# Kernel tuning notes

Measured on AMD Instinct MI355X. Metric: run time of the kernel, lower is better.

The kernel has to match this reference:

```python
import jax, jax.numpy as jnp
import numpy as np

KERNEL = 3
GROUP = 8


def setup_inputs() -> dict:
    key = jax.random.key(0)
    k1, k2 = jax.random.split(key)
    x = jax.random.normal(k1, (8, 64, 256, 256), dtype=jnp.float32)
    # 1x1 conv weight (out=group*k^2, in=dim), kaiming-ish scale
    conv_w = jax.random.normal(k2, (GROUP * KERNEL ** 2, 64), dtype=jnp.float32) * 0.1
    return {"x": x, "conv_w": conv_w}


def reference(x, conv_w):
    k, g = KERNEL, GROUP
    n, c, h, w = x.shape
    cg = c // g
    pad = k // 2

    # GAP -> 1x1 conv -> tanh : per-sample, per-group k*k dynamic filter
    gap = x.mean(axis=(2, 3))                                   # (n, c)
    filt = jnp.einsum('nc,oc->no', gap, conv_w)                 # (n, g*k*k)
    filt = jnp.tanh(filt).reshape(n, g, k * k)                  # (n, g, k*k)

    xp = jnp.pad(x, ((0, 0), (0, 0), (pad, pad), (pad, pad)), mode='reflect')
    out = jnp.zeros((n, g, cg, h, w), dtype=x.dtype)
    for i in range(k):          # small fixed kernel loop (unrolled under jit)
        for j in range(k):
            patch = xp[:, :, i:i + h, j:j + w].reshape(n, g, cg, h, w)
            wij = filt[:, :, i * k + j][:, :, None, None, None]  # (n,g,1,1,1)
            out = out + patch * wij
    return out.reshape(n, c, h, w) + x
```

## Files before the change

### kernel.cpp

```cpp
#include <hip/hip_runtime.h>

#define N 8
#define C 64
#define H 256
#define W 256
#define G 8
#define CG 8
#define KK 9
#define HW (H*W)

__global__ __launch_bounds__(256) void gap_kernel(const float* __restrict__ x,
                                                  float* __restrict__ gap) {
    const int nc = blockIdx.x;
    const float4* x4 = (const float4*)(x + (size_t)nc * HW);
    float s = 0.f;
    for (int i = threadIdx.x; i < HW / 4; i += 256) {
        float4 v = x4[i];
        s += (v.x + v.y) + (v.z + v.w);
    }
    #pragma unroll
    for (int off = 32; off > 0; off >>= 1)
        s += __shfl_down(s, off, 64);
    __shared__ float red[4];
    const int wave = threadIdx.x >> 6;
    const int lane = threadIdx.x & 63;
    if (lane == 0) red[wave] = s;
    __syncthreads();
    if (threadIdx.x == 0) {
        float t = (red[0] + red[1]) + (red[2] + red[3]);
        gap[nc] = t * (1.0f / (float)HW);
    }
}

__global__ __launch_bounds__(256) void filt_kernel(const float* __restrict__ gap,
                                                   const float* __restrict__ conv_w,
                                                   float* __restrict__ filt) {
    const int idx = blockIdx.x * 256 + threadIdx.x;
    if (idx >= N * G * KK) return;
    const int n = idx / (G * KK);
    const int o = idx - n * (G * KK);
    const float* gp = gap + n * C;
    const float* wp = conv_w + o * C;
    float s = 0.f;
    #pragma unroll
    for (int c = 0; c < C; ++c) s += gp[c] * wp[c];
    filt[idx] = tanhf(s);
}

__global__ __launch_bounds__(256) void dynconv_kernel(const float* __restrict__ x,
                                                      const float* __restrict__ filt,
                                                      float* __restrict__ out) {
    const int bid = blockIdx.x;
    const int rowblk = bid & (H / 4 - 1);
    const int nc = bid >> 6;
    const int n = nc >> 6;
    const int c = nc & (C - 1);
    const int g = c >> 3;

    const float* f = filt + ((size_t)n * G + g) * KK;
    const float f00 = f[0], f01 = f[1], f02 = f[2];
    const float f10 = f[3], f11 = f[4], f12 = f[5];
    const float f20 = f[6], f21 = f[7], f22 = f[8];

    const int tid = threadIdx.x;
    const int lrow = tid >> 6;
    const int wq = (tid & 63) * 4;
    const int hrow = rowblk * 4 + lrow;

    const float* xc = x + (size_t)nc * HW;
    int hm = hrow - 1; if (hm < 0) hm = 1;
    int hp = hrow + 1; if (hp >= H) hp = H - 2;

    const float* rm = xc + (size_t)hm * W;
    const float* rc = xc + (size_t)hrow * W;
    const float* rp = xc + (size_t)hp * W;

    float vm[6], vc[6], vp[6];
    {
        float4 a = *(const float4*)(rm + wq);
        vm[1] = a.x; vm[2] = a.y; vm[3] = a.z; vm[4] = a.w;
        vm[0] = (wq == 0) ? rm[1] : rm[wq - 1];
        vm[5] = (wq == W - 4) ? rm[W - 2] : rm[wq + 4];
    }
    {
        float4 a = *(const float4*)(rc + wq);
        vc[1] = a.x; vc[2] = a.y; vc[3] = a.z; vc[4] = a.w;
        vc[0] = (wq == 0) ? rc[1] : rc[wq - 1];
        vc[5] = (wq == W - 4) ? rc[W - 2] : rc[wq + 4];
    }
    {
        float4 a = *(const float4*)(rp + wq);
        vp[1] = a.x; vp[2] = a.y; vp[3] = a.z; vp[4] = a.w;
        vp[0] = (wq == 0) ? rp[1] : rp[wq - 1];
        vp[5] = (wq == W - 4) ? rp[W - 2] : rp[wq + 4];
    }

    float o4[4];
    #pragma unroll
    for (int k = 0; k < 4; ++k) {
        float acc = vc[k + 1];
        acc += f00 * vm[k] + f01 * vm[k + 1] + f02 * vm[k + 2];
        acc += f10 * vc[k] + f11 * vc[k + 1] + f12 * vc[k + 2];
        acc += f20 * vp[k] + f21 * vp[k + 1] + f22 * vp[k + 2];
        o4[k] = acc;
    }

    float4 r;
    r.x = o4[0]; r.y = o4[1]; r.z = o4[2]; r.w = o4[3];
    *(float4*)(out + (size_t)nc * HW + (size_t)hrow * W + wq) = r;
}

extern "C" void kernel_launch(void* const* d_in, const int* in_sizes, int n_in,
                              void* d_out, int out_size, void* d_ws, size_t ws_size,
                              hipStream_t stream) {
    const float* x      = (const float*)d_in[0];
    const float* conv_w = (const float*)d_in[1];
    float* out = (float*)d_out;

    float* gap  = (float*)d_ws;
    float* filt = (float*)d_ws + 512;

    gap_kernel<<<N * C, 256, 0, stream>>>(x, gap);
    filt_kernel<<<(N * G * KK + 255) / 256, 256, 0, stream>>>(gap, conv_w, filt);
    dynconv_kernel<<<N * C * (H / 4), 256, 0, stream>>>(x, filt, out);
}
```

Before: 284.0 us.

## Stream rows per wave with register reuse and shuffle halos in dynconv

The depthwise dynamic-filter kernel now has each wave walk 16 consecutive rows, keeping the previous two rows in registers so each input row is loaded about once instead of three times. Horizontal halo values come from wave shuffles instead of extra scalar global loads. Outputs use nontemporal stores to avoid polluting cache. The GAP reduction kernel moves to 1024-thread blocks with an unrolled loop for more memory parallelism. The trade-off is fewer blocks and more serial work per wave, which reduces the parallelism available to hide latency.

```diff
diff --git a/kernel.cpp b/kernel.cpp
--- a/kernel.cpp
+++ b/kernel.cpp
@@ -9,25 +9,30 @@
 #define KK 9
 #define HW (H*W)
 
-__global__ __launch_bounds__(256) void gap_kernel(const float* __restrict__ x,
-                                                  float* __restrict__ gap) {
+typedef float nfloat4 __attribute__((ext_vector_type(4)));
+
+__global__ __launch_bounds__(1024) void gap_kernel(const float* __restrict__ x,
+                                                   float* __restrict__ gap) {
     const int nc = blockIdx.x;
     const float4* x4 = (const float4*)(x + (size_t)nc * HW);
     float s = 0.f;
-    for (int i = threadIdx.x; i < HW / 4; i += 256) {
+    #pragma unroll 8
+    for (int i = threadIdx.x; i < HW / 4; i += 1024) {
         float4 v = x4[i];
         s += (v.x + v.y) + (v.z + v.w);
     }
     #pragma unroll
     for (int off = 32; off > 0; off >>= 1)
         s += __shfl_down(s, off, 64);
-    __shared__ float red[4];
+    __shared__ float red[16];
     const int wave = threadIdx.x >> 6;
     const int lane = threadIdx.x & 63;
     if (lane == 0) red[wave] = s;
     __syncthreads();
     if (threadIdx.x == 0) {
-        float t = (red[0] + red[1]) + (red[2] + red[3]);
+        float t = 0.f;
+        #pragma unroll
+        for (int wv = 0; wv < 16; ++wv) t += red[wv];
         gap[nc] = t * (1.0f / (float)HW);
     }
 }
@@ -47,12 +52,22 @@
     filt[idx] = tanhf(s);
 }
 
+__device__ __forceinline__ void load_row(const float* __restrict__ xc, int rr,
+                                         int lane, float4& v, float& l, float& r) {
+    rr = (rr < 0) ? 1 : (rr >= H ? H - 2 : rr);
+    v = *(const float4*)(xc + (size_t)rr * W + lane * 4);
+    const float lu = __shfl_up(v.w, 1, 64);
+    const float rd = __shfl_down(v.x, 1, 64);
+    l = (lane == 0) ? v.y : lu;
+    r = (lane == 63) ? v.z : rd;
+}
+
 __global__ __launch_bounds__(256) void dynconv_kernel(const float* __restrict__ x,
                                                       const float* __restrict__ filt,
                                                       float* __restrict__ out) {
     const int bid = blockIdx.x;
-    const int rowblk = bid & (H / 4 - 1);
-    const int nc = bid >> 6;
+    const int rb = bid & 3;
+    const int nc = bid >> 2;
     const int n = nc >> 6;
     const int c = nc & (C - 1);
     const int g = c >> 3;
@@ -62,52 +77,40 @@
     const float f10 = f[3], f11 = f[4], f12 = f[5];
     const float f20 = f[6], f21 = f[7], f22 = f[8];
 
-    const int tid = threadIdx.x;
-    const int lrow = tid >> 6;
-    const int wq = (tid & 63) * 4;
-    const int hrow = rowblk * 4 + lrow;
+    const int wave = threadIdx.x >> 6;
+    const int lane = threadIdx.x & 63;
+    const int base = rb * 64 + wave * 16;
 
     const float* xc = x + (size_t)nc * HW;
-    int hm = hrow - 1; if (hm < 0) hm = 1;
-    int hp = hrow + 1; if (hp >= H) hp = H - 2;
+    float* oc = out + (size_t)nc * HW;
 
-    const float* rm = xc + (size_t)hm * W;
-    const float* rc = xc + (size_t)hrow * W;
-    const float* rp = xc + (size_t)hp * W;
+    float4 a4, b4, c4;
+    float al, ar, bl, br, cl, cr;
+    load_row(xc, base - 1, lane, a4, al, ar);
+    load_row(xc, base,     lane, b4, bl, br);
 
-    float vm[6], vc[6], vp[6];
-    {
-        float4 a = *(const float4*)(rm + wq);
-        vm[1] = a.x; vm[2] = a.y; vm[3] = a.z; vm[4] = a.w;
-        vm[0] = (wq == 0) ? rm[1] : rm[wq - 1];
-        vm[5] = (wq == W - 4) ? rm[W - 2] : rm[wq + 4];
+    #pragma unroll 4
+    for (int i = 0; i < 16; ++i) {
+        load_row(xc, base + i + 1, lane, c4, cl, cr);
+
+        const float am[6] = {al, a4.x, a4.y, a4.z, a4.w, ar};
+        const float bm[6] = {bl, b4.x, b4.y, b4.z, b4.w, br};
+        const float cm[6] = {cl, c4.x, c4.y, c4.z, c4.w, cr};
+
+        nfloat4 o;
+        #pragma unroll
+        for (int k = 0; k < 4; ++k) {
+            float acc = bm[k + 1];
+            acc += f00 * am[k] + f01 * am[k + 1] + f02 * am[k + 2];
+            acc += f10 * bm[k] + f11 * bm[k + 1] + f12 * bm[k + 2];
+            acc += f20 * cm[k] + f21 * cm[k + 1] + f22 * cm[k + 2];
+            o[k] = acc;
+        }
+        __builtin_nontemporal_store(o, (nfloat4*)(oc + (size_t)(base + i) * W + lane * 4));
+
+        a4 = b4; al = bl; ar = br;
+        b4 = c4; bl = cl; br = cr;
     }
-    {
-        float4 a = *(const float4*)(rc + wq);
-        vc[1] = a.x; vc[2] = a.y; vc[3] = a.z; vc[4] = a.w;
-        vc[0] = (wq == 0) ? rc[1] : rc[wq - 1];
-        vc[5] = (wq == W - 4) ? rc[W - 2] : rc[wq + 4];
-    }
-    {
-        float4 a = *(const float4*)(rp + wq);
-        vp[1] = a.x; vp[2] = a.y; vp[3] = a.z; vp[4] = a.w;
-        vp[0] = (wq == 0) ? rp[1] : rp[wq - 1];
-        vp[5] = (wq == W - 4) ? rp[W - 2] : rp[wq + 4];
-    }
-
-    float o4[4];
-    #pragma unroll
-    for (int k = 0; k < 4; ++k) {
-        float acc = vc[k + 1];
-        acc += f00 * vm[k] + f01 * vm[k + 1] + f02 * vm[k + 2];
-        acc += f10 * vc[k] + f11 * vc[k + 1] + f12 * vc[k + 2];
-        acc += f20 * vp[k] + f21 * vp[k + 1] + f22 * vp[k + 2];
-        o4[k] = acc;
-    }
-
-    float4 r;
-    r.x = o4[0]; r.y = o4[1]; r.z = o4[2]; r.w = o4[3];
-    *(float4*)(out + (size_t)nc * HW + (size_t)hrow * W + wq) = r;
 }
 
 extern "C" void kernel_launch(void* const* d_in, const int* in_sizes, int n_in,
@@ -120,7 +123,7 @@
     float* gap  = (float*)d_ws;
     float* filt = (float*)d_ws + 512;
 
-    gap_kernel<<<N * C, 256, 0, stream>>>(x, gap);
+    gap_kernel<<<N * C, 1024, 0, stream>>>(x, gap);
     filt_kernel<<<(N * G * KK + 255) / 256, 256, 0, stream>>>(gap, conv_w, filt);
-    dynconv_kernel<<<N * C * (H / 4), 256, 0, stream>>>(x, filt, out);
+    dynconv_kernel<<<N * C * (H / 64), 256, 0, stream>>>(x, filt, out);
 }
```

Measured after the change: 253.7 us. -10.7%, faster.
